# Performance work log

Measured on AMD Instinct MI355X. Metric: run time of the kernel, lower is better.

## Reference

```python
import jax, jax.numpy as jnp
import numpy as np

N_NODES = 65536
IN_FEAT = 512
OUT_FEAT = 256
N_REL = 3
N_EDGES = 500000
NEG_SLOPE = 0.2  # DGL GATConv default
EPS = 1e-9


def setup_inputs() -> dict:
    key = jax.random.key(0)
    ks = jax.random.split(key, 7)
    h = jax.random.normal(ks[0], (N_NODES, IN_FEAT), dtype=jnp.float32)
    # Glorot-ish scaling keeps attention logits in a sane range
    W = jax.random.normal(ks[1], (N_REL, IN_FEAT, OUT_FEAT), dtype=jnp.float32) / np.sqrt(IN_FEAT)
    attn_l = jax.random.normal(ks[2], (N_REL, OUT_FEAT), dtype=jnp.float32) / np.sqrt(OUT_FEAT)
    attn_r = jax.random.normal(ks[3], (N_REL, OUT_FEAT), dtype=jnp.float32) / np.sqrt(OUT_FEAT)
    b = jnp.zeros((N_REL, OUT_FEAT), dtype=jnp.float32)
    src = jax.random.randint(ks[4], (N_REL, N_EDGES), 0, N_NODES, dtype=jnp.int32)
    dst = jax.random.randint(ks[5], (N_REL, N_EDGES), 0, N_NODES, dtype=jnp.int32)
    return {"h": h, "W": W, "attn_l": attn_l, "attn_r": attn_r, "b": b, "src": src, "dst": dst}


def _gat_relation(h, W_r, al_r, ar_r, b_r, src_r, dst_r):
    n = h.shape[0]
    z = h @ W_r                                  # [N, F_out] dense projection
    el = z @ al_r                                # [N] per-node left logit
    er = z @ ar_r                                # [N] per-node right logit
    e = jax.nn.leaky_relu(el[src_r] + er[dst_r], NEG_SLOPE)  # [E]
    # edge_softmax over incoming edges of each destination node
    m = jax.ops.segment_max(e, dst_r, num_segments=n)        # [N]
    w = jnp.exp(e - m[dst_r])                                # [E]
    denom = jax.ops.segment_sum(w, dst_r, num_segments=n)    # [N]
    alpha = w / (denom[dst_r] + EPS)                         # [E]
    out = jax.ops.segment_sum(alpha[:, None] * z[src_r], dst_r, num_segments=n)
    return out + b_r


def reference(h, W, attn_l, attn_r, b, src, dst):
    n_rel = W.shape[0]
    out = jnp.zeros((h.shape[0], W.shape[2]), dtype=h.dtype)
    # HeteroGraphConv default aggregate='sum' over relations; num_heads=1 then squeeze
    for r in range(n_rel):
        out = out + _gat_relation(h, W[r], attn_l[r], attn_r[r], b[r], src[r], dst[r])
    return out
```

## Files before the change

### kernel.cpp

```cpp
#include <hip/hip_runtime.h>
#include <hip/hip_bf16.h>
#include <cstdint>
#include <cstddef>

#define N_NODES 65536
#define IN_FEAT 512
#define OUT_FEAT 256
#define N_REL 3
#define TOT_EDGES (N_REL * 500000)
#define N_EDGES 500000
#define NEG_SLOPE 0.2f
#define EPS_F 1e-9f
#define BK 64

typedef __bf16 bf16x8 __attribute__((ext_vector_type(8)));
typedef float f32x4 __attribute__((ext_vector_type(4)));

__device__ __forceinline__ void async16(const void* g, void* l) {
    __builtin_amdgcn_global_load_lds(
        (const __attribute__((address_space(1))) unsigned int*)g,
        (__attribute__((address_space(3))) unsigned int*)l, 16, 0, 0);
}

__global__ void kInit(float* __restrict__ el, float* __restrict__ er,
                      int* __restrict__ head) {
    int i = blockIdx.x * blockDim.x + threadIdx.x;
    if (i < N_REL * N_NODES) {
        el[i] = 0.f;
        er[i] = 0.f;
        head[i] = -1;
    }
}

__global__ void kHb(const float* __restrict__ h, __bf16* __restrict__ hb) {
    int i = blockIdx.x * blockDim.x + threadIdx.x;
    const float4* src = (const float4*)h + (size_t)i * 2;
    float4 v0 = src[0], v1 = src[1];
    bf16x8 w;
    w[0] = (__bf16)v0.x; w[1] = (__bf16)v0.y; w[2] = (__bf16)v0.z; w[3] = (__bf16)v0.w;
    w[4] = (__bf16)v1.x; w[5] = (__bf16)v1.y; w[6] = (__bf16)v1.z; w[7] = (__bf16)v1.w;
    *(bf16x8*)(hb + (size_t)i * 8) = w;
}

__global__ __launch_bounds__(256) void kWt(const float* __restrict__ W, __bf16* __restrict__ Wt) {
    __shared__ float tile[64][65];
    int b = blockIdx.x;
    int r = b >> 5;
    int kt = (b >> 2) & 7;
    int nt = b & 3;
    int k0 = kt * 64, n0 = nt * 64;
    int t = threadIdx.x;
    int trow = t >> 6, tcol = t & 63;
    const float* Wr = W + (size_t)r * IN_FEAT * OUT_FEAT;
#pragma unroll
    for (int p = 0; p < 16; p++) {
        int k = p * 4 + trow;
        tile[k][tcol] = Wr[(size_t)(k0 + k) * OUT_FEAT + n0 + tcol];
    }
    __syncthreads();
    __bf16* Wtr = Wt + (size_t)r * OUT_FEAT * IN_FEAT;
#pragma unroll
    for (int p = 0; p < 16; p++) {
        int n = p * 4 + trow;
        Wtr[(size_t)(n0 + n) * IN_FEAT + k0 + tcol] = (__bf16)tile[tcol][n];
    }
}

__global__ __launch_bounds__(256, 2) void kGemmA(
    const __bf16* __restrict__ hb, const __bf16* __restrict__ Wt,
    const float* __restrict__ attn_l, const float* __restrict__ attn_r,
    __bf16* __restrict__ z, float* __restrict__ el, float* __restrict__ er) {
    __shared__ __bf16 Al[128 * BK];
    __shared__ __bf16 Bl[256 * BK];
    const int r = blockIdx.y;
    const int t = threadIdx.x;
    const int lane = t & 63;
    const int wave = t >> 6;
    const int wm = wave >> 1, wn = wave & 1;
    const int colL = lane & 15, quad = lane >> 4;
    const int m_base = blockIdx.x * 128;

    const __bf16* WtR = Wt + (size_t)r * OUT_FEAT * IN_FEAT;

    f32x4 acc[4][8];
#pragma unroll
    for (int mt = 0; mt < 4; mt++)
#pragma unroll
        for (int nt = 0; nt < 8; nt++) acc[mt][nt] = (f32x4){0.f, 0.f, 0.f, 0.f};

    for (int k0 = 0; k0 < IN_FEAT; k0 += BK) {
        if (k0) __syncthreads();
#pragma unroll
        for (int i = 0; i < 8; i++) {
            int s = i * 256 + t;
            int n = s >> 3, cp = s & 7, cs = cp ^ (n & 7);
            const __bf16* g = WtR + (size_t)n * IN_FEAT + k0 + cs * 8;
            __bf16* l = Bl + (size_t)(i * 256 + (wave << 6)) * 8;
            async16(g, l);
        }
#pragma unroll
        for (int i = 0; i < 4; i++) {
            int s = i * 256 + t;
            int row = s >> 3, cp = s & 7, cs = cp ^ (row & 7);
            const __bf16* g = hb + (size_t)(m_base + row) * IN_FEAT + k0 + cs * 8;
            __bf16* l = Al + (size_t)(i * 256 + (wave << 6)) * 8;
            async16(g, l);
        }
        __syncthreads();
#pragma unroll
        for (int kk = 0; kk < 2; kk++) {
            const int cbase = kk * 4 + quad;
            bf16x8 af[4], bfr[8];
#pragma unroll
            for (int mt = 0; mt < 4; mt++) {
                int row = wm * 64 + mt * 16 + colL;
                int cp = cbase ^ (row & 7);
                af[mt] = *(const bf16x8*)(Al + (size_t)((row << 3) + cp) * 8);
            }
#pragma unroll
            for (int nt = 0; nt < 8; nt++) {
                int n = wn * 128 + nt * 16 + colL;
                int cp = cbase ^ (n & 7);
                bfr[nt] = *(const bf16x8*)(Bl + (size_t)((n << 3) + cp) * 8);
            }
#pragma unroll
            for (int mt = 0; mt < 4; mt++)
#pragma unroll
                for (int nt = 0; nt < 8; nt++)
                    acc[mt][nt] = __builtin_amdgcn_mfma_f32_16x16x32_bf16(
                        af[mt], bfr[nt], acc[mt][nt], 0, 0, 0);
        }
    }

    const float* alv = attn_l + r * OUT_FEAT;
    const float* arv = attn_r + r * OUT_FEAT;
    __bf16* zr = z + (size_t)r * N_NODES * OUT_FEAT;
    float elp[4][4], erp[4][4];
#pragma unroll
    for (int mt = 0; mt < 4; mt++)
#pragma unroll
        for (int q = 0; q < 4; q++) { elp[mt][q] = 0.f; erp[mt][q] = 0.f; }
#pragma unroll
    for (int mt = 0; mt < 4; mt++) {
#pragma unroll
        for (int nt = 0; nt < 8; nt++) {
            int c = wn * 128 + nt * 16 + colL;
            float al = alv[c], ar = arv[c];
#pragma unroll
            for (int q = 0; q < 4; q++) {
                float v = acc[mt][nt][q];
                int row = m_base + wm * 64 + mt * 16 + quad * 4 + q;
                zr[(size_t)row * OUT_FEAT + c] = (__bf16)v;
                elp[mt][q] += v * al;
                erp[mt][q] += v * ar;
            }
        }
    }
#pragma unroll
    for (int mt = 0; mt < 4; mt++)
#pragma unroll
        for (int q = 0; q < 4; q++) {
#pragma unroll
            for (int off = 1; off < 16; off <<= 1) {
                elp[mt][q] += __shfl_xor(elp[mt][q], off, 64);
                erp[mt][q] += __shfl_xor(erp[mt][q], off, 64);
            }
        }
    if (colL == 0) {
#pragma unroll
        for (int mt = 0; mt < 4; mt++)
#pragma unroll
            for (int q = 0; q < 4; q++) {
                int row = m_base + wm * 64 + mt * 16 + quad * 4 + q;
                atomicAdd(el + r * N_NODES + row, elp[mt][q]);
                atomicAdd(er + r * N_NODES + row, erp[mt][q]);
            }
    }
}

__global__ __launch_bounds__(256) void kGemmC(
    const float* __restrict__ h, const __bf16* __restrict__ Wt,
    const float* __restrict__ attn_l, const float* __restrict__ attn_r,
    __bf16* __restrict__ z, float* __restrict__ el, float* __restrict__ er) {
    __shared__ __bf16 Al[128 * BK];
    __shared__ __bf16 Bl[256 * BK];
    const int r = blockIdx.y;
    const int t = threadIdx.x;
    const int lane = t & 63;
    const int wave = t >> 6;
    const int wm = wave >> 1, wn = wave & 1;
    const int colL = lane & 15, quad = lane >> 4;
    const int m_base = blockIdx.x * 128;
    const __bf16* WtR = Wt + (size_t)r * OUT_FEAT * IN_FEAT;

    f32x4 acc[4][8];
#pragma unroll
    for (int mt = 0; mt < 4; mt++)
#pragma unroll
        for (int nt = 0; nt < 8; nt++) acc[mt][nt] = (f32x4){0.f, 0.f, 0.f, 0.f};

    for (int k0 = 0; k0 < IN_FEAT; k0 += BK) {
        if (k0) __syncthreads();
#pragma unroll
        for (int i = 0; i < 8; i++) {
            int s = i * 256 + t;
            int n = s >> 3, cp = s & 7, cs = cp ^ (n & 7);
            const __bf16* g = WtR + (size_t)n * IN_FEAT + k0 + cs * 8;
            __bf16* l = Bl + (size_t)(i * 256 + (wave << 6)) * 8;
            async16(g, l);
        }
#pragma unroll
        for (int i = 0; i < 4; i++) {
            int s = i * 256 + t;
            int row = s >> 3, cp = s & 7, cs = cp ^ (row & 7);
            const float* g = h + (size_t)(m_base + row) * IN_FEAT + k0 + cs * 8;
            float4 v0 = ((const float4*)g)[0];
            float4 v1 = ((const float4*)g)[1];
            bf16x8 w;
            w[0] = (__bf16)v0.x; w[1] = (__bf16)v0.y; w[2] = (__bf16)v0.z; w[3] = (__bf16)v0.w;
            w[4] = (__bf16)v1.x; w[5] = (__bf16)v1.y; w[6] = (__bf16)v1.z; w[7] = (__bf16)v1.w;
            *(bf16x8*)(Al + (size_t)s * 8) = w;
        }
        __syncthreads();
#pragma unroll
        for (int kk = 0; kk < 2; kk++) {
            const int cbase = kk * 4 + quad;
            bf16x8 af[4], bfr[8];
#pragma unroll
            for (int mt = 0; mt < 4; mt++) {
                int row = wm * 64 + mt * 16 + colL;
                int cp = cbase ^ (row & 7);
                af[mt] = *(const bf16x8*)(Al + (size_t)((row << 3) + cp) * 8);
            }
#pragma unroll
            for (int nt = 0; nt < 8; nt++) {
                int n = wn * 128 + nt * 16 + colL;
                int cp = cbase ^ (n & 7);
                bfr[nt] = *(const bf16x8*)(Bl + (size_t)((n << 3) + cp) * 8);
            }
#pragma unroll
            for (int mt = 0; mt < 4; mt++)
#pragma unroll
                for (int nt = 0; nt < 8; nt++)
                    acc[mt][nt] = __builtin_amdgcn_mfma_f32_16x16x32_bf16(
                        af[mt], bfr[nt], acc[mt][nt], 0, 0, 0);
        }
    }
    const float* alv = attn_l + r * OUT_FEAT;
    const float* arv = attn_r + r * OUT_FEAT;
    __bf16* zr = z + (size_t)r * N_NODES * OUT_FEAT;
    float elp[4][4], erp[4][4];
#pragma unroll
    for (int mt = 0; mt < 4; mt++)
#pragma unroll
        for (int q = 0; q < 4; q++) { elp[mt][q] = 0.f; erp[mt][q] = 0.f; }
#pragma unroll
    for (int mt = 0; mt < 4; mt++) {
#pragma unroll
        for (int nt = 0; nt < 8; nt++) {
            int c = wn * 128 + nt * 16 + colL;
            float al = alv[c], ar = arv[c];
#pragma unroll
            for (int q = 0; q < 4; q++) {
                float v = acc[mt][nt][q];
                int row = m_base + wm * 64 + mt * 16 + quad * 4 + q;
                zr[(size_t)row * OUT_FEAT + c] = (__bf16)v;
                elp[mt][q] += v * al;
                erp[mt][q] += v * ar;
            }
        }
    }
#pragma unroll
    for (int mt = 0; mt < 4; mt++)
#pragma unroll
        for (int q = 0; q < 4; q++) {
#pragma unroll
            for (int off = 1; off < 16; off <<= 1) {
                elp[mt][q] += __shfl_xor(elp[mt][q], off, 64);
                erp[mt][q] += __shfl_xor(erp[mt][q], off, 64);
            }
        }
    if (colL == 0) {
#pragma unroll
        for (int mt = 0; mt < 4; mt++)
#pragma unroll
            for (int q = 0; q < 4; q++) {
                int row = m_base + wm * 64 + mt * 16 + quad * 4 + q;
                atomicAdd(el + r * N_NODES + row, elp[mt][q]);
                atomicAdd(er + r * N_NODES + row, erp[mt][q]);
            }
    }
}

__global__ void kLink(const int* __restrict__ dst, const int* __restrict__ srcArr,
                      int* __restrict__ head, int2* __restrict__ next2) {
    int i = blockIdx.x * blockDim.x + threadIdx.x;
    if (i >= TOT_EDGES) return;
    int r = i / N_EDGES;
    int d = dst[i];
    int prev = atomicExch(head + r * N_NODES + d, i);
    next2[i] = make_int2(prev, srcArr[i]);
}

__global__ __launch_bounds__(192) void kAgg(
    const __bf16* __restrict__ z, const int* __restrict__ head,
    const int2* __restrict__ next2,
    const float* __restrict__ el, const float* __restrict__ er,
    const float* __restrict__ bias, float* __restrict__ out) {
    __shared__ float cm[6][256];
    const int t = threadIdx.x;
    const int wv = t >> 6;
    const int lane = t & 63;
    const int half = lane >> 5;
    const int l = lane & 31;
    const int hw = wv * 2 + half;
    const int nl = (hw >= 3) ? 1 : 0;
    const int r = hw - nl * 3;
    const int node = blockIdx.x * 2 + nl;
    const int idx = r * N_NODES + node;

    const float erv = er[idx];
    const float* elr = el + r * N_NODES;
    const uint4* zrel = (const uint4*)(z + (size_t)r * N_NODES * OUT_FEAT);

    float p0 = 0.f, p1 = 0.f, p2 = 0.f, p3 = 0.f;
    float p4 = 0.f, p5 = 0.f, p6 = 0.f, p7 = 0.f;
    float wsum = 0.f;
    int cur = head[idx];
    while (cur >= 0) {
        int2 ns = next2[cur];
        int s = ns.y;
        float x = elr[s] + erv;
        x = x > 0.f ? x : NEG_SLOPE * x;
        float w = __expf(x);
        uint4 v = zrel[(size_t)s * 32 + l];
        wsum += w;
        p0 += w * __uint_as_float(v.x << 16);
        p1 += w * __uint_as_float(v.x & 0xFFFF0000u);
        p2 += w * __uint_as_float(v.y << 16);
        p3 += w * __uint_as_float(v.y & 0xFFFF0000u);
        p4 += w * __uint_as_float(v.z << 16);
        p5 += w * __uint_as_float(v.z & 0xFFFF0000u);
        p6 += w * __uint_as_float(v.w << 16);
        p7 += w * __uint_as_float(v.w & 0xFFFF0000u);
        cur = ns.x;
    }
    float invd = 1.f / (wsum + EPS_F);
    float* cr = &cm[hw][l * 8];
    *(float4*)cr       = make_float4(p0 * invd, p1 * invd, p2 * invd, p3 * invd);
    *(float4*)(cr + 4) = make_float4(p4 * invd, p5 * invd, p6 * invd, p7 * invd);
    __syncthreads();

    if (r == 0) {
        const int c = l * 8;
        const float* r0 = &cm[nl * 3 + 0][c];
        const float* r1 = &cm[nl * 3 + 1][c];
        const float* r2 = &cm[nl * 3 + 2][c];
        const float* b0 = bias + c;
        const float* b1 = bias + OUT_FEAT + c;
        const float* b2 = bias + 2 * OUT_FEAT + c;
        float f0 = r0[0] + r1[0] + r2[0] + b0[0] + b1[0] + b2[0];
        float f1 = r0[1] + r1[1] + r2[1] + b0[1] + b1[1] + b2[1];
        float f2 = r0[2] + r1[2] + r2[2] + b0[2] + b1[2] + b2[2];
        float f3 = r0[3] + r1[3] + r2[3] + b0[3] + b1[3] + b2[3];
        float f4 = r0[4] + r1[4] + r2[4] + b0[4] + b1[4] + b2[4];
        float f5 = r0[5] + r1[5] + r2[5] + b0[5] + b1[5] + b2[5];
        float f6 = r0[6] + r1[6] + r2[6] + b0[6] + b1[6] + b2[6];
        float f7 = r0[7] + r1[7] + r2[7] + b0[7] + b1[7] + b2[7];
        float* orow = out + (size_t)node * OUT_FEAT + c;
        *(float4*)orow       = make_float4(f0, f1, f2, f3);
        *(float4*)(orow + 4) = make_float4(f4, f5, f6, f7);
    }
}

extern "C" void kernel_launch(void* const* d_in, const int* in_sizes, int n_in,
                              void* d_out, int out_size, void* d_ws, size_t ws_size,
                              hipStream_t stream) {
    const float* h      = (const float*)d_in[0];
    const float* W      = (const float*)d_in[1];
    const float* attn_l = (const float*)d_in[2];
    const float* attn_r = (const float*)d_in[3];
    const float* bias   = (const float*)d_in[4];
    const int*   src    = (const int*)d_in[5];
    const int*   dst    = (const int*)d_in[6];
    float* out = (float*)d_out;
    char* ws = (char*)d_ws;

    const bool useHb = ws_size >= (size_t)190000000;
    size_t off_b = 0;
    auto alloc = [&](size_t bytes) {
        size_t o = off_b;
        off_b = (off_b + bytes + 255) & ~(size_t)255;
        return o;
    };
    size_t oZ    = alloc((size_t)N_REL * N_NODES * OUT_FEAT * 2);
    size_t oHB   = useHb ? alloc((size_t)N_NODES * IN_FEAT * 2) : 0;
    size_t oWT   = alloc((size_t)N_REL * OUT_FEAT * IN_FEAT * 2);
    size_t oEL   = alloc((size_t)N_REL * N_NODES * 4);
    size_t oER   = alloc((size_t)N_REL * N_NODES * 4);
    size_t oHEAD = alloc((size_t)N_REL * N_NODES * 4);
    size_t oNEXT = alloc((size_t)TOT_EDGES * 8);

    __bf16* z    = (__bf16*)(ws + oZ);
    __bf16* hb   = (__bf16*)(ws + oHB);
    __bf16* Wt   = (__bf16*)(ws + oWT);
    float*  el   = (float*)(ws + oEL);
    float*  er   = (float*)(ws + oER);
    int*    head = (int*)(ws + oHEAD);
    int2*   next2 = (int2*)(ws + oNEXT);

    kInit<<<(N_REL * N_NODES + 255) / 256, 256, 0, stream>>>(el, er, head);
    kWt<<<96, 256, 0, stream>>>(W, Wt);
    kLink<<<(TOT_EDGES + 255) / 256, 256, 0, stream>>>(dst, src, head, next2);
    if (useHb) {
        kHb<<<(N_NODES * IN_FEAT / 8 + 255) / 256, 256, 0, stream>>>(h, hb);
        kGemmA<<<dim3(N_NODES / 128, N_REL), 256, 0, stream>>>(hb, Wt, attn_l, attn_r, z, el, er);
    } else {
        kGemmC<<<dim3(N_NODES / 128, N_REL), 256, 0, stream>>>(h, Wt, attn_l, attn_r, z, el, er);
    }
    kAgg<<<N_NODES / 2, 192, 0, stream>>>(z, head, next2, el, er, bias, out);
}
```

Before: 521.2 us.

## Merge prep kernels into one launch and retile projection GEMM to 128x128

```diff
diff --git a/kernel.cpp b/kernel.cpp
--- a/kernel.cpp
+++ b/kernel.cpp
@@ -22,76 +22,77 @@
         (__attribute__((address_space(3))) unsigned int*)l, 16, 0, 0);
 }
 
-__global__ void kInit(float* __restrict__ el, float* __restrict__ er,
-                      int* __restrict__ head) {
-    int i = blockIdx.x * blockDim.x + threadIdx.x;
-    if (i < N_REL * N_NODES) {
+__global__ __launch_bounds__(256) void kPrep(
+    const float* __restrict__ W, const float* __restrict__ h,
+    __bf16* __restrict__ Wt, __bf16* __restrict__ hb,
+    float* __restrict__ el, float* __restrict__ er, int* __restrict__ head,
+    int useHb) {
+    __shared__ float tile[64][65];
+    const int b = blockIdx.x;
+    const int t = threadIdx.x;
+    if (b < 768) {
+        int i = b * 256 + t;
         el[i] = 0.f;
         er[i] = 0.f;
         head[i] = -1;
-    }
-}
-
-__global__ void kHb(const float* __restrict__ h, __bf16* __restrict__ hb) {
-    int i = blockIdx.x * blockDim.x + threadIdx.x;
-    const float4* src = (const float4*)h + (size_t)i * 2;
-    float4 v0 = src[0], v1 = src[1];
-    bf16x8 w;
-    w[0] = (__bf16)v0.x; w[1] = (__bf16)v0.y; w[2] = (__bf16)v0.z; w[3] = (__bf16)v0.w;
-    w[4] = (__bf16)v1.x; w[5] = (__bf16)v1.y; w[6] = (__bf16)v1.z; w[7] = (__bf16)v1.w;
-    *(bf16x8*)(hb + (size_t)i * 8) = w;
-}
-
-__global__ __launch_bounds__(256) void kWt(const float* __restrict__ W, __bf16* __restrict__ Wt) {
-    __shared__ float tile[64][65];
-    int b = blockIdx.x;
-    int r = b >> 5;
-    int kt = (b >> 2) & 7;
-    int nt = b & 3;
-    int k0 = kt * 64, n0 = nt * 64;
-    int t = threadIdx.x;
-    int trow = t >> 6, tcol = t & 63;
-    const float* Wr = W + (size_t)r * IN_FEAT * OUT_FEAT;
-#pragma unroll
-    for (int p = 0; p < 16; p++) {
-        int k = p * 4 + trow;
-        tile[k][tcol] = Wr[(size_t)(k0 + k) * OUT_FEAT + n0 + tcol];
-    }
-    __syncthreads();
-    __bf16* Wtr = Wt + (size_t)r * OUT_FEAT * IN_FEAT;
-#pragma unroll
-    for (int p = 0; p < 16; p++) {
-        int n = p * 4 + trow;
-        Wtr[(size_t)(n0 + n) * IN_FEAT + k0 + tcol] = (__bf16)tile[tcol][n];
-    }
-}
-
-__global__ __launch_bounds__(256, 2) void kGemmA(
+    } else if (b < 864) {
+        int b2 = b - 768;
+        int r = b2 >> 5;
+        int kt = (b2 >> 2) & 7;
+        int nt = b2 & 3;
+        int k0 = kt * 64, n0 = nt * 64;
+        int trow = t >> 6, tcol = t & 63;
+        const float* Wr = W + (size_t)r * IN_FEAT * OUT_FEAT;
+#pragma unroll
+        for (int p = 0; p < 16; p++) {
+            int k = p * 4 + trow;
+            tile[k][tcol] = Wr[(size_t)(k0 + k) * OUT_FEAT + n0 + tcol];
+        }
+        __syncthreads();
+        __bf16* Wtr = Wt + (size_t)r * OUT_FEAT * IN_FEAT;
+#pragma unroll
+        for (int p = 0; p < 16; p++) {
+            int n = p * 4 + trow;
+            Wtr[(size_t)(n0 + n) * IN_FEAT + k0 + tcol] = (__bf16)tile[tcol][n];
+        }
+    } else if (useHb) {
+        size_t i = (size_t)(b - 864) * 256 + t;
+        const float4* src = (const float4*)h + i * 2;
+        float4 v0 = src[0], v1 = src[1];
+        bf16x8 w;
+        w[0] = (__bf16)v0.x; w[1] = (__bf16)v0.y; w[2] = (__bf16)v0.z; w[3] = (__bf16)v0.w;
+        w[4] = (__bf16)v1.x; w[5] = (__bf16)v1.y; w[6] = (__bf16)v1.z; w[7] = (__bf16)v1.w;
+        *(bf16x8*)(hb + i * 8) = w;
+    }
+}
+
+__global__ __launch_bounds__(256, 3) void kGemmA(
     const __bf16* __restrict__ hb, const __bf16* __restrict__ Wt,
     const float* __restrict__ attn_l, const float* __restrict__ attn_r,
     __bf16* __restrict__ z, float* __restrict__ el, float* __restrict__ er) {
     __shared__ __bf16 Al[128 * BK];
-    __shared__ __bf16 Bl[256 * BK];
-    const int r = blockIdx.y;
+    __shared__ __bf16 Bl[128 * BK];
+    const int r = blockIdx.z;
     const int t = threadIdx.x;
     const int lane = t & 63;
     const int wave = t >> 6;
     const int wm = wave >> 1, wn = wave & 1;
     const int colL = lane & 15, quad = lane >> 4;
-    const int m_base = blockIdx.x * 128;
-
-    const __bf16* WtR = Wt + (size_t)r * OUT_FEAT * IN_FEAT;
-
-    f32x4 acc[4][8];
-#pragma unroll
-    for (int mt = 0; mt < 4; mt++)
-#pragma unroll
-        for (int nt = 0; nt < 8; nt++) acc[mt][nt] = (f32x4){0.f, 0.f, 0.f, 0.f};
+    const int m_base = blockIdx.y * 128;
+    const int n_base = blockIdx.x * 128;
+
+    const __bf16* WtR = Wt + (size_t)r * OUT_FEAT * IN_FEAT + (size_t)n_base * IN_FEAT;
+
+    f32x4 acc[4][4];
+#pragma unroll
+    for (int mt = 0; mt < 4; mt++)
+#pragma unroll
+        for (int nt = 0; nt < 4; nt++) acc[mt][nt] = (f32x4){0.f, 0.f, 0.f, 0.f};
 
     for (int k0 = 0; k0 < IN_FEAT; k0 += BK) {
         if (k0) __syncthreads();
 #pragma unroll
-        for (int i = 0; i < 8; i++) {
+        for (int i = 0; i < 4; i++) {
             int s = i * 256 + t;
             int n = s >> 3, cp = s & 7, cs = cp ^ (n & 7);
             const __bf16* g = WtR + (size_t)n * IN_FEAT + k0 + cs * 8;
@@ -110,7 +111,7 @@
 #pragma unroll
         for (int kk = 0; kk < 2; kk++) {
             const int cbase = kk * 4 + quad;
-            bf16x8 af[4], bfr[8];
+            bf16x8 af[4], bfr[4];
 #pragma unroll
             for (int mt = 0; mt < 4; mt++) {
                 int row = wm * 64 + mt * 16 + colL;
@@ -118,15 +119,15 @@
                 af[mt] = *(const bf16x8*)(Al + (size_t)((row << 3) + cp) * 8);
             }
 #pragma unroll
-            for (int nt = 0; nt < 8; nt++) {
-                int n = wn * 128 + nt * 16 + colL;
+            for (int nt = 0; nt < 4; nt++) {
+                int n = wn * 64 + nt * 16 + colL;
                 int cp = cbase ^ (n & 7);
                 bfr[nt] = *(const bf16x8*)(Bl + (size_t)((n << 3) + cp) * 8);
             }
 #pragma unroll
             for (int mt = 0; mt < 4; mt++)
 #pragma unroll
-                for (int nt = 0; nt < 8; nt++)
+                for (int nt = 0; nt < 4; nt++)
                     acc[mt][nt] = __builtin_amdgcn_mfma_f32_16x16x32_bf16(
                         af[mt], bfr[nt], acc[mt][nt], 0, 0, 0);
         }
@@ -143,8 +144,8 @@
 #pragma unroll
     for (int mt = 0; mt < 4; mt++) {
 #pragma unroll
-        for (int nt = 0; nt < 8; nt++) {
-            int c = wn * 128 + nt * 16 + colL;
+        for (int nt = 0; nt < 4; nt++) {
+            int c = n_base + wn * 64 + nt * 16 + colL;
             float al = alv[c], ar = arv[c];
 #pragma unroll
             for (int q = 0; q < 4; q++) {
@@ -409,12 +410,10 @@
     int*    head = (int*)(ws + oHEAD);
     int2*   next2 = (int2*)(ws + oNEXT);
 
-    kInit<<<(N_REL * N_NODES + 255) / 256, 256, 0, stream>>>(el, er, head);
-    kWt<<<96, 256, 0, stream>>>(W, Wt);
+    kPrep<<<17248, 256, 0, stream>>>(W, h, Wt, hb, el, er, head, useHb ? 1 : 0);
     kLink<<<(TOT_EDGES + 255) / 256, 256, 0, stream>>>(dst, src, head, next2);
     if (useHb) {
-        kHb<<<(N_NODES * IN_FEAT / 8 + 255) / 256, 256, 0, stream>>>(h, hb);
-        kGemmA<<<dim3(N_NODES / 128, N_REL), 256, 0, stream>>>(hb, Wt, attn_l, attn_r, z, el, er);
+        kGemmA<<<dim3(2, 512, 3), 256, 0, stream>>>(hb, Wt, attn_l, attn_r, z, el, er);
     } else {
         kGemmC<<<dim3(N_NODES / 128, N_REL), 256, 0, stream>>>(h, Wt, attn_l, attn_r, z, el, er);
     }
```

After: 527.5 us. Within noise of the previous version (+1.2%).
